# Performance work log

Hardware: AMD Instinct MI355X
Metric: run time of the kernel (lower is better)

Reference implementation:

```python
import jax, jax.numpy as jnp
import numpy as np

D_IN_NUM = 16
D_IN_CAT = 16
D_OUT = 10
DIM = 512
N_FREQ = 32
FREQ_SCALE = 0.01
D_EMB = 48
TEMP = 1.0
CHUNK = 5000


def setup_inputs() -> dict:
    key = jax.random.key(0)
    ks = jax.random.split(key, 10)
    B, N = 1024, 40000
    d_in_total = D_IN_NUM * D_EMB + D_IN_CAT
    return {
        "x_num": jax.random.uniform(ks[0], (B, D_IN_NUM), dtype=jnp.float32),
        "x_cat": jax.random.uniform(ks[1], (B, D_IN_CAT), dtype=jnp.float32),
        "y": jax.random.randint(ks[2], (B,), 0, D_OUT),
        "candidate_x_num": jax.random.uniform(ks[3], (N, D_IN_NUM), dtype=jnp.float32),
        "candidate_x_cat": jax.random.uniform(ks[4], (N, D_IN_CAT), dtype=jnp.float32),
        "candidate_y": jax.random.randint(ks[5], (N,), 0, D_OUT),
        "frequencies": FREQ_SCALE * jax.random.normal(ks[6], (D_IN_NUM, N_FREQ), dtype=jnp.float32),
        "lin_w": 0.05 * jax.random.normal(ks[7], (2 * N_FREQ, D_EMB), dtype=jnp.float32),
        "lin_b": jnp.zeros((D_EMB,), dtype=jnp.float32),
        "enc_w": 0.02 * jax.random.normal(ks[8], (d_in_total, DIM), dtype=jnp.float32),
        "enc_b": jnp.zeros((DIM,), dtype=jnp.float32),
    }


def _plr_encode(x_num, x_cat, frequencies, lin_w, lin_b, enc_w, enc_b):
    # PLR 'lite' embedding: [B, F] -> [B, F, 2*n_freq] -> [B, F, d_emb]
    t = 2.0 * jnp.pi * frequencies[None] * x_num[:, :, None]        # [B,F,n_freq]
    feats = jnp.concatenate([jnp.cos(t), jnp.sin(t)], axis=-1)       # [B,F,2n_freq]
    emb = jax.nn.relu(feats @ lin_w + lin_b)                         # [B,F,d_emb]
    flat = emb.reshape(emb.shape[0], -1)                             # [B,F*d_emb]
    h = jnp.concatenate([flat, x_cat], axis=1) @ enc_w + enc_b       # [B,dim]
    return h


def reference(x_num, x_cat, y, candidate_x_num, candidate_x_cat, candidate_y,
              frequencies, lin_w, lin_b, enc_w, enc_b):
    q = _plr_encode(x_num, x_cat, frequencies, lin_w, lin_b, enc_w, enc_b)           # [B,dim]
    c = _plr_encode(candidate_x_num, candidate_x_cat, frequencies, lin_w, lin_b, enc_w, enc_b)  # [N,dim]
    cand_y = jax.nn.one_hot(candidate_y, D_OUT, dtype=jnp.float32)                   # [N,K]

    # pairwise Euclidean distance (matmul form, as torch.cdist)
    d2 = (jnp.sum(q * q, axis=1, keepdims=True)
          + jnp.sum(c * c, axis=1)[None, :]
          - 2.0 * q @ c.T)
    dist = jnp.sqrt(jnp.maximum(d2, 1e-12)) / TEMP                                   # [B,N]
    exp_d = jnp.exp(-dist)                                                           # [B,N]

    # original accumulates per-5000-chunk logsumexp of exp(-d) additively
    B, N = exp_d.shape
    n_chunks = N // CHUNK
    lse = jax.nn.logsumexp(exp_d.reshape(B, n_chunks, CHUNK), axis=-1).sum(axis=-1)  # [B]
    logits = exp_d @ cand_y                                                          # [B,K]
    return jnp.log(logits) - lse[:, None]
```

## Files before the change

### kernel.cpp

```cpp
#include <hip/hip_runtime.h>
#include <math.h>

typedef __attribute__((ext_vector_type(8))) short bf16x8;
typedef __attribute__((ext_vector_type(4))) float f32x4;
typedef unsigned short u16;
typedef unsigned int u32;

#define BQ 1024
#define NCAND 40000
#define ROWS_TOT 41024
#define NF 16
#define NFREQ 32
#define DEMB 48
#define KDIM 800
#define ASTRIDE 808
#define DIM 512
#define NCLS 10
#define NCHUNK 8
#define CHUNKSZ 5000
#define CT_PER_CHUNK 40
#define NCT 320
#define PSTRIDE 136
#define TWO_PI 6.28318530717958647692f

__device__ __forceinline__ u16 f2bf(float f) {
  u32 u = __float_as_uint(f);
  u32 r = u + 0x7fffu + ((u >> 16) & 1u);
  return (u16)(r >> 16);
}
__device__ __forceinline__ float bf2f(u16 b) { return __uint_as_float(((u32)b) << 16); }
__device__ __forceinline__ u32 cvt_pk_bf16(float lo, float hi) {
  u32 r;
  asm("v_cvt_pk_bf16_f32 %0, %1, %2" : "=v"(r) : "v"(lo), "v"(hi));
  return r;
}

__global__ __launch_bounds__(256)
void k_prep(const float* __restrict__ enc_w, u16* __restrict__ enc_wT)
{
  int idx = blockIdx.x * 256 + threadIdx.x;
  if (idx >= DIM * KDIM) return;
  int n = idx / KDIM, k = idx - n * KDIM;
  u16 v = 0;
  if (k < 784) v = f2bf(enc_w[k * DIM + n]);
  enc_wT[idx] = v;
}

__global__ __launch_bounds__(256, 3)
void k_encode(const float* __restrict__ xq_num, const float* __restrict__ xq_cat,
              const float* __restrict__ xc_num, const float* __restrict__ xc_cat,
              const float* __restrict__ freq, const float* __restrict__ lin_w,
              const float* __restrict__ lin_b, const u16* __restrict__ enc_wT,
              const float* __restrict__ enc_b,
              u16* __restrict__ h_bf, float* __restrict__ norms)
{
  __shared__ u16 a_s[32 * ASTRIDE];
  __shared__ float norm_s[32];

  const int t = threadIdx.x;
  const int row0 = blockIdx.x * 32;
  const bool isq = (row0 < BQ);
  const float* __restrict__ xnum = isq ? xq_num : xc_num;
  const float* __restrict__ xcat = isq ? xq_cat : xc_cat;
  const int rbase = isq ? row0 : (row0 - BQ);

  const int wid = t >> 6, l = t & 63, hi = l >> 4, lo = l & 15;

  if (t < 32) norm_s[t] = 0.f;
  for (int i = t; i < 32 * 16; i += 256) {
    int r = i >> 4, c = i & 15;
    a_s[r * ASTRIDE + 768 + c] = f2bf(xcat[(rbase + r) * NF + c]);
  }
  for (int i = t; i < 32 * 24; i += 256) {
    int r = i / 24, c = i - r * 24;
    a_s[r * ASTRIDE + 784 + c] = 0;
  }

  {
    float fq[8];
    *(float4*)&fq[0] = *(const float4*)&freq[lo * NFREQ + hi * 8];
    *(float4*)&fq[4] = *(const float4*)&freq[lo * NFREQ + hi * 8 + 4];
    float xv[8];
#pragma unroll
    for (int mi = 0; mi < 8; ++mi)
      xv[mi] = xnum[(rbase + wid * 8 + mi) * NF + lo];

    bf16x8 lwb[2][3];
#pragma unroll
    for (int kf = 0; kf < 2; ++kf)
#pragma unroll
      for (int nf = 0; nf < 3; ++nf)
#pragma unroll
        for (int e = 0; e < 8; ++e)
          lwb[kf][nf][e] = (short)f2bf(lin_w[(kf * 32 + hi * 8 + e) * DEMB + nf * 16 + lo]);
    float lb[3];
#pragma unroll
    for (int nf = 0; nf < 3; ++nf) lb[nf] = lin_b[nf * 16 + lo];

#pragma unroll
    for (int mi = 0; mi < 8; ++mi) {
      bf16x8 ac, as_;
#pragma unroll
      for (int e = 0; e < 8; ++e) {
        float tt = TWO_PI * fq[e] * xv[mi];
        ac[e] = (short)f2bf(__cosf(tt));
        as_[e] = (short)f2bf(__sinf(tt));
      }
#pragma unroll
      for (int nf = 0; nf < 3; ++nf) {
        f32x4 ec = {0.f, 0.f, 0.f, 0.f};
        ec = __builtin_amdgcn_mfma_f32_16x16x32_bf16(ac, lwb[0][nf], ec, 0, 0, 0);
        ec = __builtin_amdgcn_mfma_f32_16x16x32_bf16(as_, lwb[1][nf], ec, 0, 0, 0);
#pragma unroll
        for (int reg = 0; reg < 4; ++reg) {
          int f = hi * 4 + reg;
          int r = wid * 8 + mi;
          float v = fmaxf(ec[reg] + lb[nf], 0.f);
          a_s[r * ASTRIDE + f * DEMB + nf * 16 + lo] = f2bf(v);
        }
      }
    }
  }
  __syncthreads();

  f32x4 acc[2][8];
#pragma unroll
  for (int mf = 0; mf < 2; ++mf)
#pragma unroll
    for (int nf = 0; nf < 8; ++nf) acc[mf][nf] = 0.f;

  for (int kt = 0; kt < KDIM / 32; ++kt) {
    bf16x8 af[2], bw[8];
#pragma unroll
    for (int mf = 0; mf < 2; ++mf)
      af[mf] = *(const bf16x8*)&a_s[(mf * 16 + lo) * ASTRIDE + kt * 32 + hi * 8];
#pragma unroll
    for (int nf = 0; nf < 8; ++nf)
      bw[nf] = *(const bf16x8*)&enc_wT[(size_t)(wid * 128 + nf * 16 + lo) * KDIM + kt * 32 + hi * 8];
#pragma unroll
    for (int mf = 0; mf < 2; ++mf)
#pragma unroll
      for (int nf = 0; nf < 8; ++nf)
        acc[mf][nf] = __builtin_amdgcn_mfma_f32_16x16x32_bf16(af[mf], bw[nf], acc[mf][nf], 0, 0, 0);
  }

  float encb_v[8];
#pragma unroll
  for (int nf = 0; nf < 8; ++nf) encb_v[nf] = enc_b[wid * 128 + nf * 16 + lo];
  float nacc[2][4];
#pragma unroll
  for (int mf = 0; mf < 2; ++mf)
#pragma unroll
    for (int r = 0; r < 4; ++r) nacc[mf][r] = 0.f;

#pragma unroll
  for (int mf = 0; mf < 2; ++mf)
#pragma unroll
    for (int nf = 0; nf < 8; ++nf)
#pragma unroll
      for (int r = 0; r < 4; ++r) {
        int m = mf * 16 + hi * 4 + r;
        int n = wid * 128 + nf * 16 + lo;
        float hv = acc[mf][nf][r] + encb_v[nf];
        u16 ub = f2bf(hv);
        h_bf[(size_t)(row0 + m) * DIM + n] = ub;
        float hb = bf2f(ub);
        nacc[mf][r] = fmaf(hb, hb, nacc[mf][r]);
      }
#pragma unroll
  for (int mf = 0; mf < 2; ++mf)
#pragma unroll
    for (int r = 0; r < 4; ++r) {
      float v = nacc[mf][r];
      v += __shfl_xor(v, 1); v += __shfl_xor(v, 2);
      v += __shfl_xor(v, 4); v += __shfl_xor(v, 8);
      if (lo == 0) atomicAdd(&norm_s[mf * 16 + hi * 4 + r], v);
    }
  __syncthreads();
  if (t < 32) norms[row0 + t] = norm_s[t];
}

__global__ __launch_bounds__(256)
void k_dist(const u16* __restrict__ h_bf, const float* __restrict__ norms,
            const int* __restrict__ cand_y,
            float* __restrict__ cls_part, float* __restrict__ lse_part)
{
  __shared__ __align__(16) u16 AB_s[12288];
  __shared__ float qn_s[64];
  __shared__ float cn_s[128];
  __shared__ int cy_s[128];
  __shared__ float lse_s[64];

  u16* A_s = AB_s;
  u16* B_s = AB_s + 8192;
  u16* P_s = AB_s;

  const int t = threadIdx.x;
  const int bx = blockIdx.x;
  const int chunk = bx / CT_PER_CHUNK;
  const int ctl = bx - chunk * CT_PER_CHUNK;
  const int cand0 = chunk * CHUNKSZ + ctl * 128;
  const int cend = chunk * CHUNKSZ + CHUNKSZ;
  const int q0 = blockIdx.y * 64;

  if (t < 64) { lse_s[t] = 0.f; qn_s[t] = norms[q0 + t]; }
  if (t < 128) {
    int j = cand0 + t; if (j > cend - 1) j = cend - 1;
    cn_s[t] = norms[BQ + j];
    cy_s[t] = cand_y[j];
  }

  const int wid = t >> 6, l = t & 63, hi = l >> 4, lo = l & 15;
  const int wm = wid & 1, wn = wid >> 1;

  f32x4 acc[4][2];
#pragma unroll
  for (int mi = 0; mi < 4; ++mi)
#pragma unroll
    for (int ni = 0; ni < 2; ++ni) acc[mi][ni] = 0.f;

  for (int kt = 0; kt < DIM / 64; ++kt) {
    __syncthreads();
#pragma unroll
    for (int p = 0; p < 4; ++p) {
      int idx = p * 256 + t;
      int lrow = idx >> 3, slot = idx & 7;
      int crow = cand0 + lrow; if (crow > cend - 1) crow = cend - 1;
      float4 v = *(const float4*)&h_bf[(size_t)(BQ + crow) * DIM + kt * 64 + slot * 8];
      *(float4*)&A_s[lrow * 64 + ((((u32)slot * 16) ^ (((u32)lrow & 7) << 4)) >> 1)] = v;
    }
#pragma unroll
    for (int p = 0; p < 2; ++p) {
      int idx = p * 256 + t;
      int qrow = idx >> 3, slot = idx & 7;
      float4 v = *(const float4*)&h_bf[(size_t)(q0 + qrow) * DIM + kt * 64 + slot * 8];
      *(float4*)&B_s[qrow * 64 + ((((u32)slot * 16) ^ (((u32)qrow & 7) << 4)) >> 1)] = v;
    }
    __syncthreads();
#pragma unroll
    for (int ks = 0; ks < 2; ++ks) {
      bf16x8 af[4], bq[2];
#pragma unroll
      for (int mi = 0; mi < 4; ++mi) {
        int row = wm * 64 + mi * 16 + lo;
        int byt = (hi * 16 + ks * 64) ^ ((row & 7) << 4);
        af[mi] = *(const bf16x8*)&A_s[row * 64 + (byt >> 1)];
      }
#pragma unroll
      for (int ni = 0; ni < 2; ++ni) {
        int row = wn * 32 + ni * 16 + lo;
        int byt = (hi * 16 + ks * 64) ^ ((row & 7) << 4);
        bq[ni] = *(const bf16x8*)&B_s[row * 64 + (byt >> 1)];
      }
#pragma unroll
      for (int mi = 0; mi < 4; ++mi)
#pragma unroll
        for (int ni = 0; ni < 2; ++ni)
          acc[mi][ni] = __builtin_amdgcn_mfma_f32_16x16x32_bf16(af[mi], bq[ni], acc[mi][ni], 0, 0, 0);
    }
  }

  float qv[2];
#pragma unroll
  for (int ni = 0; ni < 2; ++ni) qv[ni] = qn_s[wn * 32 + ni * 16 + lo];

  u32 pk[4][2][2];
  float lacc[2] = {0.f, 0.f};
#pragma unroll
  for (int mi = 0; mi < 4; ++mi)
#pragma unroll
    for (int ni = 0; ni < 2; ++ni) {
      float ev[4];
#pragma unroll
      for (int r = 0; r < 4; ++r) {
        int crow = wm * 64 + mi * 16 + hi * 4 + r;
        bool valid = (cand0 + crow) < cend;
        float d2 = fmaf(-2.f, acc[mi][ni][r], cn_s[crow] + qv[ni]);
        float dist = __builtin_amdgcn_sqrtf(fmaxf(d2, 1e-12f));
        float e = valid ? __expf(-dist) : 0.f;
        ev[r] = e;
        lacc[ni] += valid ? __expf(e) : 0.f;
      }
      pk[mi][ni][0] = cvt_pk_bf16(ev[0], ev[1]);
      pk[mi][ni][1] = cvt_pk_bf16(ev[2], ev[3]);
    }

#pragma unroll
  for (int ni = 0; ni < 2; ++ni) {
    float v = lacc[ni];
    v += __shfl_xor(v, 16); v += __shfl_xor(v, 32);
    if (hi == 0) atomicAdd(&lse_s[wn * 32 + ni * 16 + lo], v);
  }

  __syncthreads();
#pragma unroll
  for (int mi = 0; mi < 4; ++mi)
#pragma unroll
    for (int ni = 0; ni < 2; ++ni) {
      int q = wn * 32 + ni * 16 + lo;
      int j0 = wm * 64 + mi * 16 + hi * 4;
      *(uint2*)&P_s[q * PSTRIDE + j0] = make_uint2(pk[mi][ni][0], pk[mi][ni][1]);
    }
  __syncthreads();

  {
    f32x4 accc = {0.f, 0.f, 0.f, 0.f};
    const u16* Prow = P_s + (wn * 32 + wm * 16 + lo) * PSTRIDE;
#pragma unroll
    for (int ks = 0; ks < 4; ++ks) {
      bf16x8 af = *(const bf16x8*)(Prow + ks * 32 + hi * 8);
      bf16x8 yb;
#pragma unroll
      for (int e = 0; e < 8; ++e) {
        int j = ks * 32 + hi * 8 + e;
        yb[e] = (short)((cy_s[j] == lo) ? 0x3F80 : 0);
      }
      accc = __builtin_amdgcn_mfma_f32_16x16x32_bf16(af, yb, accc, 0, 0, 0);
    }
    if (lo < NCLS) {
#pragma unroll
      for (int reg = 0; reg < 4; ++reg) {
        int qq = wn * 32 + wm * 16 + hi * 4 + reg;
        cls_part[((size_t)bx * BQ + (q0 + qq)) * NCLS + lo] = accc[reg];
      }
    }
  }

  if (t < 64) lse_part[(size_t)bx * BQ + q0 + t] = lse_s[t];
}

__global__ __launch_bounds__(320)
void k_final(const float* __restrict__ cls_part, const float* __restrict__ lse_part,
             float* __restrict__ out)
{
  __shared__ float cls_sum[NCLS];
  __shared__ float ch_sum[NCHUNK];
  const int t = threadIdx.x;
  const int b = blockIdx.x;
  if (t < NCLS) cls_sum[t] = 0.f;
  if (t < NCHUNK) ch_sum[t] = 0.f;
  __syncthreads();

  float cs[NCLS];
#pragma unroll
  for (int c = 0; c < NCLS; ++c) cs[c] = cls_part[((size_t)t * BQ + b) * NCLS + c];
  float ls = lse_part[(size_t)t * BQ + b];
  atomicAdd(&ch_sum[t / CT_PER_CHUNK], ls);
#pragma unroll
  for (int c = 0; c < NCLS; ++c) {
    float w = cs[c];
    w += __shfl_xor(w, 1); w += __shfl_xor(w, 2); w += __shfl_xor(w, 4);
    w += __shfl_xor(w, 8); w += __shfl_xor(w, 16); w += __shfl_xor(w, 32);
    if ((t & 63) == 0) atomicAdd(&cls_sum[c], w);
  }
  __syncthreads();
  if (t < NCLS) {
    float lse = 0.f;
#pragma unroll
    for (int ch = 0; ch < NCHUNK; ++ch) lse += logf(ch_sum[ch]);
    out[b * NCLS + t] = logf(cls_sum[t]) - lse;
  }
}

extern "C" void kernel_launch(void* const* d_in, const int* in_sizes, int n_in,
                              void* d_out, int out_size, void* d_ws, size_t ws_size,
                              hipStream_t stream)
{
  const float* xq_num = (const float*)d_in[0];
  const float* xq_cat = (const float*)d_in[1];
  const float* xc_num = (const float*)d_in[3];
  const float* xc_cat = (const float*)d_in[4];
  const int* cand_y = (const int*)d_in[5];
  const float* freq = (const float*)d_in[6];
  const float* lin_w = (const float*)d_in[7];
  const float* lin_b = (const float*)d_in[8];
  const float* enc_w = (const float*)d_in[9];
  const float* enc_b = (const float*)d_in[10];

  u16* h_bf = (u16*)d_ws;
  float* norms = (float*)((char*)d_ws + (size_t)ROWS_TOT * DIM * 2);
  float* cls_part = norms + ROWS_TOT;
  float* lse_part = cls_part + (size_t)NCT * BQ * NCLS;
  u16* enc_wT = (u16*)(lse_part + (size_t)NCT * BQ);
  float* out = (float*)d_out;

  hipLaunchKernelGGL(k_prep, dim3((DIM * KDIM + 255) / 256), dim3(256), 0, stream,
                     enc_w, enc_wT);
  hipLaunchKernelGGL(k_encode, dim3(ROWS_TOT / 32), dim3(256), 0, stream,
                     xq_num, xq_cat, xc_num, xc_cat, freq, lin_w, lin_b,
                     enc_wT, enc_b, h_bf, norms);
  hipLaunchKernelGGL(k_dist, dim3(NCT, BQ / 64), dim3(256), 0, stream,
                     h_bf, norms, cand_y, cls_part, lse_part);
  hipLaunchKernelGGL(k_final, dim3(BQ), dim3(320), 0, stream,
                     cls_part, lse_part, out);
}
```

Baseline: 206.3 us.

## Enlarge encoder tile to 64 rows with 8 waves and register double-buffering

The encoder GEMM block now handles 64 rows with 512 threads. Each wave computes a 64x64 output tile instead of 32x128, so every enc_wT fragment loaded from global memory is reused across twice as many rows. The K loop is manually unrolled with ping-pong register buffers so loads for the next K step are issued before the MFMAs of the current one. In exchange the shared-memory tile doubles to about 103 KB per block, which likely allows only one block per CU and reduces resident waves.

```diff
diff --git a/kernel.cpp b/kernel.cpp
--- a/kernel.cpp
+++ b/kernel.cpp
@@ -21,6 +21,7 @@
 #define CT_PER_CHUNK 40
 #define NCT 320
 #define PSTRIDE 136
+#define MROWS 64
 #define TWO_PI 6.28318530717958647692f
 
 __device__ __forceinline__ u16 f2bf(float f) {
@@ -46,7 +47,7 @@
   enc_wT[idx] = v;
 }
 
-__global__ __launch_bounds__(256, 3)
+__global__ __launch_bounds__(512, 2)
 void k_encode(const float* __restrict__ xq_num, const float* __restrict__ xq_cat,
               const float* __restrict__ xc_num, const float* __restrict__ xc_cat,
               const float* __restrict__ freq, const float* __restrict__ lin_w,
@@ -54,11 +55,11 @@
               const float* __restrict__ enc_b,
               u16* __restrict__ h_bf, float* __restrict__ norms)
 {
-  __shared__ u16 a_s[32 * ASTRIDE];
-  __shared__ float norm_s[32];
+  __shared__ u16 a_s[MROWS * ASTRIDE];
+  __shared__ float norm_s[MROWS];
 
   const int t = threadIdx.x;
-  const int row0 = blockIdx.x * 32;
+  const int row0 = blockIdx.x * MROWS;
   const bool isq = (row0 < BQ);
   const float* __restrict__ xnum = isq ? xq_num : xc_num;
   const float* __restrict__ xcat = isq ? xq_cat : xc_cat;
@@ -66,12 +67,12 @@
 
   const int wid = t >> 6, l = t & 63, hi = l >> 4, lo = l & 15;
 
-  if (t < 32) norm_s[t] = 0.f;
-  for (int i = t; i < 32 * 16; i += 256) {
+  if (t < MROWS) norm_s[t] = 0.f;
+  for (int i = t; i < MROWS * 16; i += 512) {
     int r = i >> 4, c = i & 15;
     a_s[r * ASTRIDE + 768 + c] = f2bf(xcat[(rbase + r) * NF + c]);
   }
-  for (int i = t; i < 32 * 24; i += 256) {
+  for (int i = t; i < MROWS * 24; i += 512) {
     int r = i / 24, c = i - r * 24;
     a_s[r * ASTRIDE + 784 + c] = 0;
   }
@@ -123,44 +124,66 @@
   }
   __syncthreads();
 
-  f32x4 acc[2][8];
-#pragma unroll
-  for (int mf = 0; mf < 2; ++mf)
-#pragma unroll
-    for (int nf = 0; nf < 8; ++nf) acc[mf][nf] = 0.f;
-
-  for (int kt = 0; kt < KDIM / 32; ++kt) {
-    bf16x8 af[2], bw[8];
-#pragma unroll
-    for (int mf = 0; mf < 2; ++mf)
-      af[mf] = *(const bf16x8*)&a_s[(mf * 16 + lo) * ASTRIDE + kt * 32 + hi * 8];
-#pragma unroll
-    for (int nf = 0; nf < 8; ++nf)
-      bw[nf] = *(const bf16x8*)&enc_wT[(size_t)(wid * 128 + nf * 16 + lo) * KDIM + kt * 32 + hi * 8];
-#pragma unroll
-    for (int mf = 0; mf < 2; ++mf)
-#pragma unroll
-      for (int nf = 0; nf < 8; ++nf)
-        acc[mf][nf] = __builtin_amdgcn_mfma_f32_16x16x32_bf16(af[mf], bw[nf], acc[mf][nf], 0, 0, 0);
-  }
-
-  float encb_v[8];
-#pragma unroll
-  for (int nf = 0; nf < 8; ++nf) encb_v[nf] = enc_b[wid * 128 + nf * 16 + lo];
-  float nacc[2][4];
-#pragma unroll
-  for (int mf = 0; mf < 2; ++mf)
+  f32x4 acc[4][4];
+#pragma unroll
+  for (int mf = 0; mf < 4; ++mf)
+#pragma unroll
+    for (int nf = 0; nf < 4; ++nf) acc[mf][nf] = 0.f;
+
+  const u16* bwbase = enc_wT + (size_t)(wid * 64 + lo) * KDIM + hi * 8;
+  const u16* asbase = a_s + lo * ASTRIDE + hi * 8;
+
+  bf16x8 afA[4], bwA[4], afB[4], bwB[4];
+
+#define LOADK(kt, af, bw)                                                     \
+  {                                                                           \
+    _Pragma("unroll")                                                         \
+    for (int nf = 0; nf < 4; ++nf)                                            \
+      bw[nf] = *(const bf16x8*)(bwbase + (size_t)nf * 16 * KDIM + (kt) * 32); \
+    _Pragma("unroll")                                                         \
+    for (int mf = 0; mf < 4; ++mf)                                            \
+      af[mf] = *(const bf16x8*)(asbase + mf * 16 * ASTRIDE + (kt) * 32);      \
+  }
+#define MFMAK(af, bw)                                                         \
+  {                                                                           \
+    _Pragma("unroll")                                                         \
+    for (int mf = 0; mf < 4; ++mf)                                            \
+      _Pragma("unroll")                                                       \
+      for (int nf = 0; nf < 4; ++nf)                                          \
+        acc[mf][nf] =                                                         \
+            __builtin_amdgcn_mfma_f32_16x16x32_bf16(af[mf], bw[nf],           \
+                                                    acc[mf][nf], 0, 0, 0);    \
+  }
+
+  LOADK(0, afA, bwA);
+#pragma unroll
+  for (int i = 0; i < 12; ++i) {
+    LOADK(2 * i + 1, afB, bwB);
+    MFMAK(afA, bwA);
+    LOADK(2 * i + 2, afA, bwA);
+    MFMAK(afB, bwB);
+  }
+  MFMAK(afA, bwA);
+#undef LOADK
+#undef MFMAK
+
+  float encb_v[4];
+#pragma unroll
+  for (int nf = 0; nf < 4; ++nf) encb_v[nf] = enc_b[wid * 64 + nf * 16 + lo];
+  float nacc[4][4];
+#pragma unroll
+  for (int mf = 0; mf < 4; ++mf)
 #pragma unroll
     for (int r = 0; r < 4; ++r) nacc[mf][r] = 0.f;
 
 #pragma unroll
-  for (int mf = 0; mf < 2; ++mf)
-#pragma unroll
-    for (int nf = 0; nf < 8; ++nf)
+  for (int mf = 0; mf < 4; ++mf)
+#pragma unroll
+    for (int nf = 0; nf < 4; ++nf)
 #pragma unroll
       for (int r = 0; r < 4; ++r) {
         int m = mf * 16 + hi * 4 + r;
-        int n = wid * 128 + nf * 16 + lo;
+        int n = wid * 64 + nf * 16 + lo;
         float hv = acc[mf][nf][r] + encb_v[nf];
         u16 ub = f2bf(hv);
         h_bf[(size_t)(row0 + m) * DIM + n] = ub;
@@ -168,7 +191,7 @@
         nacc[mf][r] = fmaf(hb, hb, nacc[mf][r]);
       }
 #pragma unroll
-  for (int mf = 0; mf < 2; ++mf)
+  for (int mf = 0; mf < 4; ++mf)
 #pragma unroll
     for (int r = 0; r < 4; ++r) {
       float v = nacc[mf][r];
@@ -177,7 +200,7 @@
       if (lo == 0) atomicAdd(&norm_s[mf * 16 + hi * 4 + r], v);
     }
   __syncthreads();
-  if (t < 32) norms[row0 + t] = norm_s[t];
+  if (t < MROWS) norms[row0 + t] = norm_s[t];
 }
 
 __global__ __launch_bounds__(256)
@@ -386,7 +409,7 @@
 
   hipLaunchKernelGGL(k_prep, dim3((DIM * KDIM + 255) / 256), dim3(256), 0, stream,
                      enc_w, enc_wT);
-  hipLaunchKernelGGL(k_encode, dim3(ROWS_TOT / 32), dim3(256), 0, stream,
+  hipLaunchKernelGGL(k_encode, dim3(ROWS_TOT / MROWS), dim3(512), 0, stream,
                      xq_num, xq_cat, xc_num, xc_cat, freq, lin_w, lin_b,
                      enc_wT, enc_b, h_bf, norms);
   hipLaunchKernelGGL(k_dist, dim3(NCT, BQ / 64), dim3(256), 0, stream,
```

Result: faster. 188.8 us (-8.5%).
